# Optimization experiments

Hardware: AMD Instinct MI355X
Metric: run time of the kernel (lower is better)

## Reference

```python
import jax, jax.numpy as jnp
import numpy as np


def setup_inputs() -> dict:
    key = jax.random.key(0)
    k1, k2, k3 = jax.random.split(key, 3)
    B, L, W, Q = 16, 4096, 1024, 4
    h = jax.random.normal(k1, (B, L, W), dtype=jnp.float32)
    mask = jax.random.randint(k2, (B, L), 0, 2).astype(jnp.bool_)  # True = masked out
    queries = jax.random.normal(k3, (Q, W), dtype=jnp.float32)
    return {"h": h, "mask": mask, "queries": queries}


def reference(h, mask, queries):
    # h: (B, L, W), mask: (B, L) bool (True = masked), queries: (Q, W)
    B, L, W = h.shape
    Q = queries.shape[0]
    scale = W ** (-0.5)
    # scores: (B, Q, L)
    attn = jnp.einsum("qw,blw->bql", queries, h) * scale
    attn = jnp.where(mask[:, None, :], -jnp.inf, attn)
    attn = jax.nn.softmax(attn, axis=-1)
    pooled = jnp.einsum("bql,blw->bqw", attn, h)  # (B, Q, W)
    return pooled.reshape(B, Q * W)
```

## Files before the change

### kernel.cpp

```cpp
#include <hip/hip_runtime.h>
#include <math.h>

#define BB 16
#define LL 4096
#define WW 1024
#define NQ 4
#define SCALE 0.03125f

__global__ __launch_bounds__(256, 2) void pool_main(
    const float* __restrict__ h,
    const int* __restrict__ mask,
    const float* __restrict__ queries,
    float* __restrict__ Opart,
    float* __restrict__ MSpart,
    int P)
{
    const int tid  = threadIdx.x;
    const int lane = tid & 63;
    const int wv   = tid >> 6;
    const int b    = blockIdx.x / P;
    const int p    = blockIdx.x % P;
    const int rpw  = LL / (P * 4);
    const int l0   = (p * 4 + wv) * rpw;

    float4 qreg[NQ][4];
#pragma unroll
    for (int q = 0; q < NQ; ++q) {
#pragma unroll
        for (int j = 0; j < 4; ++j) {
            float4 v = *reinterpret_cast<const float4*>(
                queries + q * WW + j * 256 + lane * 4);
            qreg[q][j].x = v.x * SCALE;
            qreg[q][j].y = v.y * SCALE;
            qreg[q][j].z = v.z * SCALE;
            qreg[q][j].w = v.w * SCALE;
        }
    }

    float4 o[NQ][4];
    float  m[NQ], s[NQ];
#pragma unroll
    for (int q = 0; q < NQ; ++q) {
        m[q] = -INFINITY;
        s[q] = 0.0f;
#pragma unroll
        for (int j = 0; j < 4; ++j)
            o[q][j] = make_float4(0.f, 0.f, 0.f, 0.f);
    }

    for (int g = 0; g < rpw; g += 64) {
        const int nrows = (rpw - g < 64) ? (rpw - g) : 64;
        int mv = 0;
        if (lane < nrows) mv = mask[(size_t)b * LL + l0 + g + lane];
        const unsigned long long mb = __ballot(mv != 0);

        for (int r = 0; r < nrows; ++r) {
            if ((mb >> r) & 1ull) continue;
            const float* hrow = h + ((size_t)b * LL + (l0 + g + r)) * WW;
            float4 hv[4];
#pragma unroll
            for (int j = 0; j < 4; ++j)
                hv[j] = *reinterpret_cast<const float4*>(hrow + j * 256 + lane * 4);

            float pd[NQ];
#pragma unroll
            for (int q = 0; q < NQ; ++q) {
                float acc = 0.f;
#pragma unroll
                for (int j = 0; j < 4; ++j) {
                    acc = fmaf(hv[j].x, qreg[q][j].x, acc);
                    acc = fmaf(hv[j].y, qreg[q][j].y, acc);
                    acc = fmaf(hv[j].z, qreg[q][j].z, acc);
                    acc = fmaf(hv[j].w, qreg[q][j].w, acc);
                }
                pd[q] = acc;
            }
#pragma unroll
            for (int off = 32; off > 0; off >>= 1) {
#pragma unroll
                for (int q = 0; q < NQ; ++q)
                    pd[q] += __shfl_xor(pd[q], off);
            }

#pragma unroll
            for (int q = 0; q < NQ; ++q) {
                const float sc = pd[q];
                if (sc > m[q]) {
                    const float c = __expf(m[q] - sc);
                    s[q] = s[q] * c + 1.0f;
#pragma unroll
                    for (int j = 0; j < 4; ++j) {
                        o[q][j].x = o[q][j].x * c + hv[j].x;
                        o[q][j].y = o[q][j].y * c + hv[j].y;
                        o[q][j].z = o[q][j].z * c + hv[j].z;
                        o[q][j].w = o[q][j].w * c + hv[j].w;
                    }
                    m[q] = sc;
                } else {
                    const float pp = __expf(sc - m[q]);
                    s[q] += pp;
#pragma unroll
                    for (int j = 0; j < 4; ++j) {
                        o[q][j].x = fmaf(pp, hv[j].x, o[q][j].x);
                        o[q][j].y = fmaf(pp, hv[j].y, o[q][j].y);
                        o[q][j].z = fmaf(pp, hv[j].z, o[q][j].z);
                        o[q][j].w = fmaf(pp, hv[j].w, o[q][j].w);
                    }
                }
            }
        }
    }

    __shared__ float lo[NQ][WW];
    __shared__ float lm[4][NQ];
    __shared__ float lss[4][NQ];

    if (lane == 0) {
#pragma unroll
        for (int q = 0; q < NQ; ++q) { lm[wv][q] = m[q]; lss[wv][q] = s[q]; }
    }
    for (int i = tid; i < NQ * WW; i += 256) ((float*)lo)[i] = 0.f;
    __syncthreads();

    float M[NQ], fw[NQ];
#pragma unroll
    for (int q = 0; q < NQ; ++q) {
        M[q] = fmaxf(fmaxf(lm[0][q], lm[1][q]), fmaxf(lm[2][q], lm[3][q]));
        fw[q] = (m[q] == -INFINITY) ? 0.f : __expf(m[q] - M[q]);
    }

    for (int t = 0; t < 4; ++t) {
        if (wv == t) {
#pragma unroll
            for (int q = 0; q < NQ; ++q) {
#pragma unroll
                for (int j = 0; j < 4; ++j) {
                    float* dst = &lo[q][j * 256 + lane * 4];
                    dst[0] += fw[q] * o[q][j].x;
                    dst[1] += fw[q] * o[q][j].y;
                    dst[2] += fw[q] * o[q][j].z;
                    dst[3] += fw[q] * o[q][j].w;
                }
            }
        }
        __syncthreads();
    }

    float S[NQ];
#pragma unroll
    for (int q = 0; q < NQ; ++q) {
        float acc = 0.f;
#pragma unroll
        for (int t = 0; t < 4; ++t) {
            const float mt = lm[t][q];
            if (mt != -INFINITY) acc += __expf(mt - M[q]) * lss[t][q];
        }
        S[q] = acc;
    }

    float* Ob = Opart + ((size_t)(b * P + p) * NQ) * WW;
    for (int i = tid; i < NQ * WW; i += 256) Ob[i] = ((float*)lo)[i];
    if (tid < NQ) {
        const size_t base = ((size_t)(b * P + p) * NQ + tid) * 2;
        MSpart[base]     = M[tid];
        MSpart[base + 1] = S[tid];
    }
}

__global__ __launch_bounds__(256) void pool_combine(
    const float* __restrict__ Opart,
    const float* __restrict__ MSpart,
    float* __restrict__ out,
    int P)
{
    const int b = blockIdx.x / NQ;
    const int q = blockIdx.x % NQ;
    const int tid = threadIdx.x;
    const int w = tid * 4;

    float M = -INFINITY;
    for (int i = 0; i < P; ++i)
        M = fmaxf(M, MSpart[((size_t)(b * P + i) * NQ + q) * 2]);

    float S = 0.f;
    float4 acc = make_float4(0.f, 0.f, 0.f, 0.f);
    for (int i = 0; i < P; ++i) {
        const size_t msb = ((size_t)(b * P + i) * NQ + q) * 2;
        const float mi = MSpart[msb];
        if (mi == -INFINITY) continue;
        const float f = __expf(mi - M);
        S += f * MSpart[msb + 1];
        const float4 v = *reinterpret_cast<const float4*>(
            Opart + ((size_t)(b * P + i) * NQ + q) * WW + w);
        acc.x = fmaf(f, v.x, acc.x);
        acc.y = fmaf(f, v.y, acc.y);
        acc.z = fmaf(f, v.z, acc.z);
        acc.w = fmaf(f, v.w, acc.w);
    }

    const float inv = 1.0f / S;
    float4 r;
    r.x = acc.x * inv; r.y = acc.y * inv; r.z = acc.z * inv; r.w = acc.w * inv;
    *reinterpret_cast<float4*>(out + (size_t)b * (NQ * WW) + q * WW + w) = r;
}

extern "C" void kernel_launch(void* const* d_in, const int* in_sizes, int n_in,
                              void* d_out, int out_size, void* d_ws, size_t ws_size,
                              hipStream_t stream) {
    const float* h       = (const float*)d_in[0];
    const int*   mask    = (const int*)d_in[1];
    const float* queries = (const float*)d_in[2];
    float*       out     = (float*)d_out;

    int P = 32;
    while (P > 1) {
        size_t need = (size_t)BB * P * NQ * WW * sizeof(float)
                    + (size_t)BB * P * NQ * 2 * sizeof(float);
        if (need <= ws_size) break;
        P >>= 1;
    }

    float* Opart  = (float*)d_ws;
    float* MSpart = Opart + (size_t)BB * P * NQ * WW;

    pool_main<<<dim3(BB * P), dim3(256), 0, stream>>>(h, mask, queries,
                                                      Opart, MSpart, P);
    pool_combine<<<dim3(BB * NQ), dim3(256), 0, stream>>>(Opart, MSpart, out, P);
}
```

Before: 357.6 us.

## Process four unmasked rows per iteration with batched online-softmax updates

Each wave now takes up to four unmasked rows at once by popping set bits from the valid mask, issues all their loads together, and batches the shuffle reductions. The online-softmax update becomes branch-free: the max is taken over the four rows and a single rescale is applied per group. The aim is more memory-level parallelism and fewer serialized shuffle/branch steps per row. The cost is higher register pressure (64 extra floats of h per lane) under launch_bounds(256,2), which risks spills or lower occupancy.

```diff
diff --git a/kernel.cpp b/kernel.cpp
--- a/kernel.cpp
+++ b/kernel.cpp
@@ -48,64 +48,97 @@
             o[q][j] = make_float4(0.f, 0.f, 0.f, 0.f);
     }
 
+    const float* hbase = h + (size_t)b * LL * WW;
+
     for (int g = 0; g < rpw; g += 64) {
         const int nrows = (rpw - g < 64) ? (rpw - g) : 64;
         int mv = 0;
         if (lane < nrows) mv = mask[(size_t)b * LL + l0 + g + lane];
         const unsigned long long mb = __ballot(mv != 0);
-
-        for (int r = 0; r < nrows; ++r) {
-            if ((mb >> r) & 1ull) continue;
-            const float* hrow = h + ((size_t)b * LL + (l0 + g + r)) * WW;
-            float4 hv[4];
-#pragma unroll
-            for (int j = 0; j < 4; ++j)
-                hv[j] = *reinterpret_cast<const float4*>(hrow + j * 256 + lane * 4);
-
-            float pd[NQ];
+        unsigned long long valid = ~mb;
+        if (nrows < 64) valid &= ((1ull << nrows) - 1ull);
+
+        while (valid) {
+            int r[4];
+            int vld[4];
+#pragma unroll
+            for (int k = 0; k < 4; ++k) {
+                if (valid) {
+                    r[k] = __ffsll((unsigned long long)valid) - 1;
+                    valid &= valid - 1ull;
+                    vld[k] = 1;
+                } else {
+                    r[k] = r[0];
+                    vld[k] = 0;
+                }
+            }
+
+            float4 hv[4][4];
+#pragma unroll
+            for (int k = 0; k < 4; ++k) {
+                const float* hrow = hbase + (size_t)(l0 + g + r[k]) * WW;
+#pragma unroll
+                for (int j = 0; j < 4; ++j)
+                    hv[k][j] = *reinterpret_cast<const float4*>(
+                        hrow + j * 256 + lane * 4);
+            }
+
+            float pd[4][NQ];
+#pragma unroll
+            for (int k = 0; k < 4; ++k) {
+#pragma unroll
+                for (int q = 0; q < NQ; ++q) {
+                    float acc = 0.f;
+#pragma unroll
+                    for (int j = 0; j < 4; ++j) {
+                        acc = fmaf(hv[k][j].x, qreg[q][j].x, acc);
+                        acc = fmaf(hv[k][j].y, qreg[q][j].y, acc);
+                        acc = fmaf(hv[k][j].z, qreg[q][j].z, acc);
+                        acc = fmaf(hv[k][j].w, qreg[q][j].w, acc);
+                    }
+                    pd[k][q] = acc;
+                }
+            }
+
+#pragma unroll
+            for (int off = 32; off > 0; off >>= 1) {
+#pragma unroll
+                for (int k = 0; k < 4; ++k)
+#pragma unroll
+                    for (int q = 0; q < NQ; ++q)
+                        pd[k][q] += __shfl_xor(pd[k][q], off);
+            }
+
+#pragma unroll
+            for (int k = 0; k < 4; ++k)
+                if (!vld[k])
+#pragma unroll
+                    for (int q = 0; q < NQ; ++q) pd[k][q] = -INFINITY;
+
 #pragma unroll
             for (int q = 0; q < NQ; ++q) {
-                float acc = 0.f;
+                const float bm = fmaxf(fmaxf(pd[0][q], pd[1][q]),
+                                       fmaxf(pd[2][q], pd[3][q]));
+                const float mn = fmaxf(m[q], bm);
+                const float c  = __expf(m[q] - mn);
+                float pr[4];
+#pragma unroll
+                for (int k = 0; k < 4; ++k)
+                    pr[k] = __expf(pd[k][q] - mn);
+                s[q] = s[q] * c + ((pr[0] + pr[1]) + (pr[2] + pr[3]));
+                m[q] = mn;
 #pragma unroll
                 for (int j = 0; j < 4; ++j) {
-                    acc = fmaf(hv[j].x, qreg[q][j].x, acc);
-                    acc = fmaf(hv[j].y, qreg[q][j].y, acc);
-                    acc = fmaf(hv[j].z, qreg[q][j].z, acc);
-                    acc = fmaf(hv[j].w, qreg[q][j].w, acc);
-                }
-                pd[q] = acc;
-            }
-#pragma unroll
-            for (int off = 32; off > 0; off >>= 1) {
-#pragma unroll
-                for (int q = 0; q < NQ; ++q)
-                    pd[q] += __shfl_xor(pd[q], off);
-            }
-
-#pragma unroll
-            for (int q = 0; q < NQ; ++q) {
-                const float sc = pd[q];
-                if (sc > m[q]) {
-                    const float c = __expf(m[q] - sc);
-                    s[q] = s[q] * c + 1.0f;
-#pragma unroll
-                    for (int j = 0; j < 4; ++j) {
-                        o[q][j].x = o[q][j].x * c + hv[j].x;
-                        o[q][j].y = o[q][j].y * c + hv[j].y;
-                        o[q][j].z = o[q][j].z * c + hv[j].z;
-                        o[q][j].w = o[q][j].w * c + hv[j].w;
+                    float x = o[q][j].x * c, y = o[q][j].y * c;
+                    float z = o[q][j].z * c, w = o[q][j].w * c;
+#pragma unroll
+                    for (int k = 0; k < 4; ++k) {
+                        x = fmaf(pr[k], hv[k][j].x, x);
+                        y = fmaf(pr[k], hv[k][j].y, y);
+                        z = fmaf(pr[k], hv[k][j].z, z);
+                        w = fmaf(pr[k], hv[k][j].w, w);
                     }
-                    m[q] = sc;
-                } else {
-                    const float pp = __expf(sc - m[q]);
-                    s[q] += pp;
-#pragma unroll
-                    for (int j = 0; j < 4; ++j) {
-                        o[q][j].x = fmaf(pp, hv[j].x, o[q][j].x);
-                        o[q][j].y = fmaf(pp, hv[j].y, o[q][j].y);
-                        o[q][j].z = fmaf(pp, hv[j].z, o[q][j].z);
-                        o[q][j].w = fmaf(pp, hv[j].w, o[q][j].w);
-                    }
+                    o[q][j].x = x; o[q][j].y = y; o[q][j].z = z; o[q][j].w = w;
                 }
             }
         }
```

After: 357.3 us. No clear change (-0.1%).
